# Kernel tuning notes

Measured on AMD Instinct MI355X. Metric: run time of the kernel, lower is better.

## Reference

```python
import jax, jax.numpy as jnp
import numpy as np

B, D, S, H, L = 256, 7, 32, 512, 128  # batch, tree depth, n_symbols, hidden_size, latent_size
N = 2 ** D - 1  # nodes in complete binary tree, heap order (children of i are 2i+1, 2i+2)


def _xavier(key, shape):
    lim = float(np.sqrt(6.0 / (shape[0] + shape[1])))
    return jax.random.uniform(key, shape, jnp.float32, -lim, lim)


def setup_inputs():
    key = jax.random.key(0)
    ks = jax.random.split(key, 18)
    return {
        'symbols': jax.random.randint(ks[0], (B, N), 0, S, dtype=jnp.int32),
        'eps': jax.random.normal(ks[1], (B, L), jnp.float32),
        # Encoder GRU221: gate order [r, z, n], input weights act on one-hot symbol, hidden weights on cat(h_l, h_r)
        'ewi': _xavier(ks[2], (3 * H, S)),
        'ebi': jax.random.uniform(ks[3], (3 * H,), jnp.float32, -0.05, 0.05),
        'ewh': _xavier(ks[4], (3 * H, 2 * H)),
        'ebh': jax.random.uniform(ks[5], (3 * H,), jnp.float32, -0.05, 0.05),
        'h2mu_w': _xavier(ks[6], (L, H)),
        'h2mu_b': jax.random.uniform(ks[7], (L,), jnp.float32, -0.05, 0.05),
        'h2lv_w': _xavier(ks[8], (L, H)),
        'h2lv_b': jax.random.uniform(ks[9], (L,), jnp.float32, -0.05, 0.05),
        # Decoder
        'z2h_w': _xavier(ks[10], (H, L)),
        'z2h_b': jax.random.uniform(ks[11], (H,), jnp.float32, -0.05, 0.05),
        'h2o_w': _xavier(ks[12], (S, H)),
        'h2o_b': jax.random.uniform(ks[13], (S,), jnp.float32, -0.05, 0.05),
        # Decoder GRU122: gate order [r, z, n], each gate has 2H outputs (left/right child)
        'dwi': _xavier(ks[14], (6 * H, S)),
        'dbi': jax.random.uniform(ks[15], (6 * H,), jnp.float32, -0.05, 0.05),
        'dwh': _xavier(ks[16], (6 * H, H)),
        'dbh': jax.random.uniform(ks[17], (6 * H,), jnp.float32, -0.05, 0.05),
    }


def _hvae_forward(symbols, eps, ewi, ebi, ewh, ebh, h2mu_w, h2mu_b, h2lv_w, h2lv_b,
                  z2h_w, z2h_b, h2o_w, h2o_b, dwi, dbi, dwh, dbh):
    x_all = jax.nn.one_hot(symbols, S, dtype=jnp.float32)  # [B, N, S] node targets

    # ---- Encoder: GRU221 applied bottom-up, one batched step per tree level ----
    h = jnp.zeros((B, 2 ** D, H), jnp.float32)  # (absent) children of the deepest level
    for d in range(D - 1, -1, -1):
        n_d = 2 ** d
        x = x_all[:, n_d - 1: 2 * n_d - 1]       # [B, n_d, S] level-d symbols (heap order)
        hl, hr = h[:, 0::2], h[:, 1::2]           # [B, n_d, H] left/right child hiddens
        hcat = jnp.concatenate([hl, hr], axis=-1)
        gi = x @ ewi.T + ebi                       # [B, n_d, 3H]
        gh = hcat @ ewh.T + ebh
        r = jax.nn.sigmoid(gi[..., :H] + gh[..., :H])
        zg = jax.nn.sigmoid(gi[..., H:2 * H] + gh[..., H:2 * H])
        n = jnp.tanh(gi[..., 2 * H:] + r * gh[..., 2 * H:])
        h = (1.0 - zg) * n + zg * (hl + hr) * 0.5
    root = h[:, 0]                                 # [B, H]
    mu = root @ h2mu_w.T + h2mu_b                  # [B, L]
    logvar = root @ h2lv_w.T + h2lv_b
    zlat = mu + eps * jnp.exp(0.5 * logvar)        # reparameterized sample

    # ---- Decoder: GRU122 applied top-down, one batched step per tree level ----
    hidden = (zlat @ z2h_w.T + z2h_b)[:, None, :]  # [B, 1, H] root hidden
    preds = []
    for d in range(D):
        pred = hidden @ h2o_w.T + h2o_b            # [B, 2^d, S]
        preds.append(pred)
        if d < D - 1:
            a = jax.nn.softmax(pred, axis=-1)
            gi = a @ dwi.T + dbi                    # [B, 2^d, 6H]
            gh = hidden @ dwh.T + dbh
            r = jax.nn.sigmoid(gi[..., :2 * H] + gh[..., :2 * H])
            zg = jax.nn.sigmoid(gi[..., 2 * H:4 * H] + gh[..., 2 * H:4 * H])
            n = jnp.tanh(gi[..., 4 * H:] + r * gh[..., 4 * H:])
            dh = jnp.concatenate([hidden, hidden], axis=-1)  # h.repeat(1,1,2)
            out = (1.0 - zg) * n + zg * dh          # [B, 2^d, 2H]
            # torch.split -> (left, right); interleave as next level's hiddens (heap order)
            hidden = jnp.stack([out[..., :H], out[..., H:]], axis=2).reshape(B, 2 ** (d + 1), H)
    preds = jnp.concatenate(preds, axis=1)          # [B, N, S] per-node logits, level order
    return mu, logvar, preds


def reference(symbols, eps, ewi, ebi, ewh, ebh, h2mu_w, h2mu_b, h2lv_w, h2lv_b,
              z2h_w, z2h_b, h2o_w, h2o_b, dwi, dbi, dwh, dbh):
    return _hvae_forward(symbols, eps, ewi, ebi, ewh, ebh, h2mu_w, h2mu_b, h2lv_w, h2lv_b,
                         z2h_w, z2h_b, h2o_w, h2o_b, dwi, dbi, dwh, dbh)
```

## Files before the change

kernel.cpp:

```cpp
#include <hip/hip_runtime.h>
#include <hip/hip_bf16.h>

typedef unsigned short u16;
typedef unsigned int u32;
typedef __attribute__((ext_vector_type(8))) short short8;
typedef __attribute__((ext_vector_type(4))) float f32x4;

#define WAITV(N) asm volatile("s_waitcnt vmcnt(" #N ")" ::: "memory")

__device__ __forceinline__ float sigmoidf_(float x) { return 1.0f / (1.0f + expf(-x)); }

__device__ __forceinline__ float bf2f(u16 u) {
    union { u32 i; float f; } v; v.i = ((u32)u) << 16; return v.f;
}
__device__ __forceinline__ u16 f2bf(float f) {
    union { float f; u32 i; } v; v.f = f;
    u32 lsb = (v.i >> 16) & 1u;
    v.i += 0x7fffu + lsb;
    return (u16)(v.i >> 16);
}

__device__ __forceinline__ void gload16(const u16* g, u16* l) {
    __builtin_amdgcn_global_load_lds(
        (const __attribute__((address_space(1))) u32*)g,
        (__attribute__((address_space(3))) u32*)l, 16, 0, 0);
}

__global__ __launch_bounds__(256) void cvt_bf16(const float* __restrict__ src,
                                                u16* __restrict__ dst, int n)
{
    int i = blockIdx.x * 256 + threadIdx.x;
    if (i < n) dst[i] = f2bf(src[i]);
}

__global__ __launch_bounds__(256) void onehot_k(
    const int* __restrict__ symbols, u16* __restrict__ oneh)
{
    int idx = blockIdx.x * 256 + threadIdx.x;
    int col = idx & 31;
    int row = idx >> 5;
    oneh[idx] = (col == symbols[row]) ? (u16)0x3F80 : (u16)0;
}

__global__ __launch_bounds__(256) void leaf_tab(
    const float* __restrict__ ewi, const float* __restrict__ ebi,
    const float* __restrict__ ebh, u16* __restrict__ tab)
{
    int idx = blockIdx.x * 256 + threadIdx.x;
    int c = idx & 511;
    int sym = idx >> 9;
    float r = sigmoidf_(ewi[c * 32 + sym]          + ebi[c]        + ebh[c]);
    float z = sigmoidf_(ewi[(512 + c) * 32 + sym]  + ebi[512 + c]  + ebh[512 + c]);
    float n = tanhf(    ewi[(1024 + c) * 32 + sym] + ebi[1024 + c] + r * ebh[1024 + c]);
    tab[idx] = f2bf((1.0f - z) * n);
}

__global__ __launch_bounds__(256) void enc_leaf(
    const u16* __restrict__ tab, const int* __restrict__ symbols,
    u16* __restrict__ hout)
{
    int t = blockIdx.x * 256 + threadIdx.x;
    int m = t >> 6, c0 = (t & 63) * 8;
    int sym = symbols[(m >> 6) * 127 + 63 + (m & 63)];
    *reinterpret_cast<short8*>(hout + (size_t)m * 512 + c0) =
        *reinterpret_cast<const short8*>(tab + sym * 512 + c0);
}

template<int RF>
__global__ __launch_bounds__(256, 2) void enc_tile(
    const u16* __restrict__ A, const u16* __restrict__ W,
    const u16* __restrict__ oneh, const u16* __restrict__ Wi,
    const float* __restrict__ ebi, const float* __restrict__ ebh,
    u16* __restrict__ hout, int dlog, int node_base)
{
    constexpr int BM = RF * 32;
    constexpr int NCA = BM / 64;
    constexpr int NS = 32;
    __shared__ alignas(16) u16 Als[4][BM * 32];
    __shared__ alignas(16) u16 Bls[4][192 * 32];
    const int tid  = threadIdx.x;
    const int lane = tid & 63;
    const int wid  = tid >> 6;
    const int wr = wid >> 1, wc = wid & 1;
    const int lr = lane & 15, lk = lane >> 4;
    const int m0 = blockIdx.x * BM;
    const int c0 = blockIdx.y * 64;

    size_t a_goff[NCA]; int a_loff[NCA];
#pragma unroll
    for (int j = 0; j < NCA; ++j) {
        int a = wid * NCA + j;
        int r_ = a * 16 + (lane >> 2);
        int kps = (lane & 3) ^ ((r_ >> 1) & 3);
        a_goff[j] = (size_t)(m0 + r_) * 1024 + kps * 8;
        a_loff[j] = a * 512 + lane * 8;
    }
    size_t b_goff[3]; int b_loff[3];
#pragma unroll
    for (int j = 0; j < 3; ++j) {
        int b = wid * 3 + j;
        int rr = b * 16 + (lane >> 2);
        int kps = (lane & 3) ^ ((rr >> 1) & 3);
        int grow = (rr >> 6) * 512 + c0 + (rr & 63);
        b_goff[j] = (size_t)grow * 1024 + kps * 8;
        b_loff[j] = b * 512 + lane * 8;
    }
    int a_roff[RF];
#pragma unroll
    for (int i = 0; i < RF; ++i) {
        int row = wr * (RF * 16) + i * 16 + lr;
        a_roff[i] = row * 32 + (lk ^ ((row >> 1) & 3)) * 8;
    }
    int b_roff[3][2];
#pragma unroll
    for (int s = 0; s < 3; ++s)
#pragma unroll
        for (int cf = 0; cf < 2; ++cf) {
            int row = s * 64 + wc * 32 + cf * 16 + lr;
            b_roff[s][cf] = row * 32 + (lk ^ ((row >> 1) & 3)) * 8;
        }

    f32x4 acc[4][2][RF];
#pragma unroll
    for (int s = 0; s < 4; ++s)
#pragma unroll
        for (int cf = 0; cf < 2; ++cf)
#pragma unroll
            for (int i = 0; i < RF; ++i) acc[s][cf][i] = (f32x4){0.f, 0.f, 0.f, 0.f};

    auto issue = [&](int stg) {
        const int buf = stg & 3;
        const int nk = stg * 32;
#pragma unroll
        for (int j = 0; j < NCA; ++j) gload16(A + a_goff[j] + nk, &Als[buf][a_loff[j]]);
#pragma unroll
        for (int j = 0; j < 3; ++j) gload16(W + b_goff[j] + nk, &Bls[buf][b_loff[j]]);
    };
    auto compute = [&](int buf) {
        short8 a[RF];
#pragma unroll
        for (int i = 0; i < RF; ++i)
            a[i] = *reinterpret_cast<const short8*>(&Als[buf][a_roff[i]]);
#pragma unroll
        for (int s = 0; s < 3; ++s)
#pragma unroll
            for (int cf = 0; cf < 2; ++cf) {
                short8 b = *reinterpret_cast<const short8*>(&Bls[buf][b_roff[s][cf]]);
#pragma unroll
                for (int i = 0; i < RF; ++i)
                    acc[s][cf][i] = __builtin_amdgcn_mfma_f32_16x16x32_bf16(a[i], b, acc[s][cf][i], 0, 0, 0);
            }
    };

    issue(0); issue(1); issue(2);
    for (int t = 0; t < NS - 2; ++t) {
        if constexpr (RF == 4) WAITV(10); else WAITV(8);
        __builtin_amdgcn_s_barrier();
        if (t + 3 < NS) issue(t + 3);
        compute(t & 3);
    }
    if constexpr (RF == 4) WAITV(5); else WAITV(4);
    __builtin_amdgcn_s_barrier();
    compute((NS - 2) & 3);
    WAITV(0);
    __builtin_amdgcn_s_barrier();
    compute((NS - 1) & 3);

    const int mask = (1 << dlog) - 1;
    {
        short8 oh[RF];
#pragma unroll
        for (int i = 0; i < RF; ++i) {
            int m = m0 + wr * (RF * 16) + i * 16 + lr;
            int b_ = m >> dlog, j_ = m & mask;
            oh[i] = *reinterpret_cast<const short8*>(
                oneh + (size_t)(b_ * 127 + node_base + j_) * 32 + lk * 8);
        }
#pragma unroll
        for (int s = 0; s < 3; ++s) {
            const int d = (s == 2) ? 3 : s;
#pragma unroll
            for (int cf = 0; cf < 2; ++cf) {
                short8 wb = *reinterpret_cast<const short8*>(
                    Wi + (size_t)(s * 512 + c0 + wc * 32 + cf * 16 + lr) * 32 + lk * 8);
#pragma unroll
                for (int i = 0; i < RF; ++i)
                    acc[d][cf][i] = __builtin_amdgcn_mfma_f32_16x16x32_bf16(oh[i], wb, acc[d][cf][i], 0, 0, 0);
            }
        }
    }

    float ebr[2], ebz[2], ebin[2], ebhn[2];
#pragma unroll
    for (int cf = 0; cf < 2; ++cf) {
        int c = c0 + wc * 32 + cf * 16 + lr;
        ebr[cf]  = ebi[c] + ebh[c];
        ebz[cf]  = ebi[512 + c] + ebh[512 + c];
        ebin[cf] = ebi[1024 + c];
        ebhn[cf] = ebh[1024 + c];
    }
#pragma unroll
    for (int i = 0; i < RF; ++i)
#pragma unroll
        for (int r = 0; r < 4; ++r) {
            int m = m0 + wr * (RF * 16) + i * 16 + lk * 4 + r;
#pragma unroll
            for (int cf = 0; cf < 2; ++cf) {
                int c = c0 + wc * 32 + cf * 16 + lr;
                float rr_ = sigmoidf_(acc[0][cf][i][r] + ebr[cf]);
                float zz  = sigmoidf_(acc[1][cf][i][r] + ebz[cf]);
                float nn  = tanhf(acc[3][cf][i][r] + ebin[cf] + rr_ * (acc[2][cf][i][r] + ebhn[cf]));
                float hl = bf2f(A[(size_t)m * 1024 + c]);
                float hr = bf2f(A[(size_t)m * 1024 + 512 + c]);
                hout[(size_t)m * 512 + c] = f2bf((1.0f - zz) * nn + zz * (hl + hr) * 0.5f);
            }
        }
}

__global__ __launch_bounds__(256) void mid1(
    const u16* __restrict__ root, const float* __restrict__ h2mu_w,
    const float* __restrict__ h2mu_b, const float* __restrict__ h2lv_w,
    const float* __restrict__ h2lv_b, const float* __restrict__ eps,
    float* __restrict__ zlat, float* __restrict__ out_mu,
    float* __restrict__ out_lv)
{
    int b = blockIdx.x, t = threadIdx.x;
    __shared__ float rs[512];
    rs[t]       = bf2f(root[(size_t)b * 512 + t]);
    rs[t + 256] = bf2f(root[(size_t)b * 512 + t + 256]);
    __syncthreads();
    const float* w = (t < 128) ? (h2mu_w + (size_t)t * 512) : (h2lv_w + (size_t)(t - 128) * 512);
    float acc = 0.0f;
    for (int k = 0; k < 512; ++k) acc += rs[k] * w[k];
    acc += (t < 128) ? h2mu_b[t] : h2lv_b[t - 128];
    __shared__ float vals[256];
    vals[t] = acc;
    __syncthreads();
    if (t < 128) {
        float mu = vals[t], lv = vals[t + 128];
        float zl = mu + eps[b * 128 + t] * expf(0.5f * lv);
        zlat[b * 128 + t] = zl;
        out_mu[b * 128 + t] = mu;
        out_lv[b * 128 + t] = lv;
    }
}

__global__ __launch_bounds__(512) void mid2(
    const float* __restrict__ zlat, const float* __restrict__ z2h_w,
    const float* __restrict__ z2h_b, u16* __restrict__ hidden)
{
    int b = blockIdx.x, t = threadIdx.x;
    __shared__ float zs[128];
    if (t < 128) zs[t] = zlat[b * 128 + t];
    __syncthreads();
    float acc = z2h_b[t];
    for (int k = 0; k < 128; ++k) acc += zs[k] * z2h_w[(size_t)t * 128 + k];
    hidden[(size_t)b * 512 + t] = f2bf(acc);
}

__global__ __launch_bounds__(256) void pred_mfma(
    const u16* __restrict__ hidden, const u16* __restrict__ Wo,
    const float* __restrict__ h2o_b, u16* __restrict__ aout,
    float* __restrict__ preds_out, int dlog, int node_base, int write_a)
{
    const int lane = threadIdx.x & 63;
    const int wid  = threadIdx.x >> 6;
    const int lr = lane & 15, lk = lane >> 4;
    const int m0 = blockIdx.x * 64 + wid * 16;

    f32x4 acc0 = (f32x4){0.f, 0.f, 0.f, 0.f};
    f32x4 acc1 = (f32x4){0.f, 0.f, 0.f, 0.f};
    const u16* Arow = hidden + (size_t)(m0 + lr) * 512 + lk * 8;
    const u16* B0 = Wo + (size_t)lr * 512 + lk * 8;
    const u16* B1 = Wo + (size_t)(16 + lr) * 512 + lk * 8;
#pragma unroll
    for (int k0 = 0; k0 < 512; k0 += 32) {
        short8 a  = *reinterpret_cast<const short8*>(Arow + k0);
        short8 b0 = *reinterpret_cast<const short8*>(B0 + k0);
        short8 b1 = *reinterpret_cast<const short8*>(B1 + k0);
        acc0 = __builtin_amdgcn_mfma_f32_16x16x32_bf16(a, b0, acc0, 0, 0, 0);
        acc1 = __builtin_amdgcn_mfma_f32_16x16x32_bf16(a, b1, acc1, 0, 0, 0);
    }
    const float bb0 = h2o_b[lr], bb1 = h2o_b[16 + lr];
    const int dmask = (1 << dlog) - 1;
#pragma unroll
    for (int r = 0; r < 4; ++r) {
        float p0 = acc0[r] + bb0;
        float p1 = acc1[r] + bb1;
        float mx = fmaxf(p0, p1);
#pragma unroll
        for (int off = 1; off < 16; off <<= 1) mx = fmaxf(mx, __shfl_xor(mx, off));
        float e0 = expf(p0 - mx), e1 = expf(p1 - mx);
        float s = e0 + e1;
#pragma unroll
        for (int off = 1; off < 16; off <<= 1) s += __shfl_xor(s, off);
        int m = m0 + lk * 4 + r;
        int b_ = m >> dlog, j_ = m & dmask;
        size_t o = (size_t)(b_ * 127 + node_base + j_) * 32;
        preds_out[o + lr] = p0;
        preds_out[o + 16 + lr] = p1;
        if (write_a) {
            float inv = 1.0f / s;
            aout[(size_t)m * 32 + lr]      = f2bf(e0 * inv);
            aout[(size_t)m * 32 + 16 + lr] = f2bf(e1 * inv);
        }
    }
}

template<int RF>
__global__ __launch_bounds__(256, 2) void dec_tile(
    const u16* __restrict__ Hin, const u16* __restrict__ aB,
    const u16* __restrict__ Wh, const u16* __restrict__ Wi,
    const float* __restrict__ dbh, const float* __restrict__ dbi,
    u16* __restrict__ Hout)
{
    constexpr int BM = RF * 32;
    constexpr int NCA = BM / 64;
    constexpr int NS = 16;
    __shared__ alignas(16) u16 Als[4][BM * 32];
    __shared__ alignas(16) u16 Bls[4][192 * 32];
    const int tid  = threadIdx.x;
    const int lane = tid & 63;
    const int wid  = tid >> 6;
    const int wr = wid >> 1, wc = wid & 1;
    const int lr = lane & 15, lk = lane >> 4;
    const int m0 = blockIdx.x * BM;
    const int c0 = blockIdx.y * 64;

    size_t a_goff[NCA]; int a_loff[NCA];
#pragma unroll
    for (int j = 0; j < NCA; ++j) {
        int a = wid * NCA + j;
        int r_ = a * 16 + (lane >> 2);
        int kps = (lane & 3) ^ ((r_ >> 1) & 3);
        a_goff[j] = (size_t)(m0 + r_) * 512 + kps * 8;
        a_loff[j] = a * 512 + lane * 8;
    }
    size_t b_goff[3]; int b_loff[3];
#pragma unroll
    for (int j = 0; j < 3; ++j) {
        int b = wid * 3 + j;
        int rr = b * 16 + (lane >> 2);
        int kps = (lane & 3) ^ ((rr >> 1) & 3);
        int grow = (rr >> 6) * 1024 + c0 + (rr & 63);
        b_goff[j] = (size_t)grow * 512 + kps * 8;
        b_loff[j] = b * 512 + lane * 8;
    }
    int a_roff[RF];
#pragma unroll
    for (int i = 0; i < RF; ++i) {
        int row = wr * (RF * 16) + i * 16 + lr;
        a_roff[i] = row * 32 + (lk ^ ((row >> 1) & 3)) * 8;
    }
    int b_roff[3][2];
#pragma unroll
    for (int s = 0; s < 3; ++s)
#pragma unroll
        for (int cf = 0; cf < 2; ++cf) {
            int row = s * 64 + wc * 32 + cf * 16 + lr;
            b_roff[s][cf] = row * 32 + (lk ^ ((row >> 1) & 3)) * 8;
        }

    f32x4 acc[4][2][RF];
#pragma unroll
    for (int s = 0; s < 4; ++s)
#pragma unroll
        for (int cf = 0; cf < 2; ++cf)
#pragma unroll
            for (int i = 0; i < RF; ++i) acc[s][cf][i] = (f32x4){0.f, 0.f, 0.f, 0.f};

    auto issue = [&](int stg) {
        const int buf = stg & 3;
        const int nk = stg * 32;
#pragma unroll
        for (int j = 0; j < NCA; ++j) gload16(Hin + a_goff[j] + nk, &Als[buf][a_loff[j]]);
#pragma unroll
        for (int j = 0; j < 3; ++j) gload16(Wh + b_goff[j] + nk, &Bls[buf][b_loff[j]]);
    };
    auto compute = [&](int buf) {
        short8 a[RF];
#pragma unroll
        for (int i = 0; i < RF; ++i)
            a[i] = *reinterpret_cast<const short8*>(&Als[buf][a_roff[i]]);
#pragma unroll
        for (int s = 0; s < 3; ++s)
#pragma unroll
            for (int cf = 0; cf < 2; ++cf) {
                short8 b = *reinterpret_cast<const short8*>(&Bls[buf][b_roff[s][cf]]);
#pragma unroll
                for (int i = 0; i < RF; ++i)
                    acc[s][cf][i] = __builtin_amdgcn_mfma_f32_16x16x32_bf16(a[i], b, acc[s][cf][i], 0, 0, 0);
            }
    };

    issue(0); issue(1); issue(2);
    for (int t = 0; t < NS - 2; ++t) {
        if constexpr (RF == 4) WAITV(10); else WAITV(8);
        __builtin_amdgcn_s_barrier();
        if (t + 3 < NS) issue(t + 3);
        compute(t & 3);
    }
    if constexpr (RF == 4) WAITV(5); else WAITV(4);
    __builtin_amdgcn_s_barrier();
    compute((NS - 2) & 3);
    WAITV(0);
    __builtin_amdgcn_s_barrier();
    compute((NS - 1) & 3);

#pragma unroll
    for (int i = 0; i < RF; ++i) {
        short8 aw = *reinterpret_cast<const short8*>(
            aB + (size_t)(m0 + wr * (RF * 16) + i * 16 + lr) * 32 + lk * 8);
#pragma unroll
        for (int s = 0; s < 3; ++s) {
            const int d = (s == 2) ? 3 : s;
#pragma unroll
            for (int cf = 0; cf < 2; ++cf) {
                short8 b = *reinterpret_cast<const short8*>(
                    Wi + (size_t)(s * 1024 + c0 + wc * 32 + cf * 16 + lr) * 32 + lk * 8);
                acc[d][cf][i] = __builtin_amdgcn_mfma_f32_16x16x32_bf16(aw, b, acc[d][cf][i], 0, 0, 0);
            }
        }
    }

#pragma unroll
    for (int i = 0; i < RF; ++i)
#pragma unroll
        for (int r = 0; r < 4; ++r) {
            int m = m0 + wr * (RF * 16) + i * 16 + lk * 4 + r;
#pragma unroll
            for (int cf = 0; cf < 2; ++cf) {
                int c = c0 + wc * 32 + cf * 16 + lr;
                float rr_ = sigmoidf_(acc[0][cf][i][r] + dbh[c]        + dbi[c]);
                float zz  = sigmoidf_(acc[1][cf][i][r] + dbh[1024 + c] + dbi[1024 + c]);
                float nn  = tanhf(acc[3][cf][i][r] + dbi[2048 + c] + rr_ * (acc[2][cf][i][r] + dbh[2048 + c]));
                float hid = bf2f(Hin[(size_t)m * 512 + (c & 511)]);
                Hout[(size_t)m * 1024 + c] = f2bf((1.0f - zz) * nn + zz * hid);
            }
        }
}

extern "C" void kernel_launch(void* const* d_in, const int* in_sizes, int n_in,
                              void* d_out, int out_size, void* d_ws, size_t ws_size,
                              hipStream_t stream) {
    const int*   symbols = (const int*)  d_in[0];
    const float* eps     = (const float*)d_in[1];
    const float* ewi     = (const float*)d_in[2];
    const float* ebi     = (const float*)d_in[3];
    const float* ewh     = (const float*)d_in[4];
    const float* ebh     = (const float*)d_in[5];
    const float* h2mu_w  = (const float*)d_in[6];
    const float* h2mu_b  = (const float*)d_in[7];
    const float* h2lv_w  = (const float*)d_in[8];
    const float* h2lv_b  = (const float*)d_in[9];
    const float* z2h_w   = (const float*)d_in[10];
    const float* z2h_b   = (const float*)d_in[11];
    const float* h2o_w   = (const float*)d_in[12];
    const float* h2o_b   = (const float*)d_in[13];
    const float* dwi     = (const float*)d_in[14];
    const float* dbi     = (const float*)d_in[15];
    const float* dwh     = (const float*)d_in[16];
    const float* dbh     = (const float*)d_in[17];

    float* out    = (float*)d_out;
    float* out_mu = out;
    float* out_lv = out + 256 * 128;
    float* out_pr = out + 2 * 256 * 128;

    u16* bufL  = (u16*)d_ws;
    u16* bufS  = bufL  + (size_t)16384 * 512;
    u16* ewh_b = bufS  + (size_t)8192 * 512;
    u16* dwh_b = ewh_b + (size_t)1536 * 1024;
    u16* dwi_b = dwh_b + (size_t)3072 * 512;
    u16* ewi_b = dwi_b + (size_t)3072 * 32;
    u16* wo_b  = ewi_b + (size_t)1536 * 32;
    u16* ltab  = wo_b  + (size_t)32 * 512;
    u16* oneh  = ltab  + (size_t)32 * 512;
    u16* aBuf  = oneh  + (size_t)32512 * 32;
    float* zlat = (float*)(aBuf + (size_t)8192 * 32);

    cvt_bf16<<<(1572864 + 255) / 256, 256, 0, stream>>>(ewh, ewh_b, 1572864);
    cvt_bf16<<<(1572864 + 255) / 256, 256, 0, stream>>>(dwh, dwh_b, 1572864);
    cvt_bf16<<<(98304 + 255) / 256, 256, 0, stream>>>(dwi, dwi_b, 98304);
    cvt_bf16<<<(49152 + 255) / 256, 256, 0, stream>>>(ewi, ewi_b, 49152);
    cvt_bf16<<<(16384 + 255) / 256, 256, 0, stream>>>(h2o_w, wo_b, 16384);
    onehot_k<<<(32512 * 32) / 256, 256, 0, stream>>>(symbols, oneh);
    leaf_tab<<<64, 256, 0, stream>>>(ewi, ebi, ebh, ltab);

    enc_leaf<<<4096, 256, 0, stream>>>(ltab, symbols, bufL);
    const u16* src = bufL;
    u16*       dst = bufS;
    for (int d = 5; d >= 0; --d) {
        int M = 256 << d;
        if (M >= 8192)
            enc_tile<4><<<dim3(M / 128, 8), 256, 0, stream>>>(src, ewh_b, oneh, ewi_b,
                                                              ebi, ebh, dst, d, (1 << d) - 1);
        else
            enc_tile<2><<<dim3(M / 64, 8), 256, 0, stream>>>(src, ewh_b, oneh, ewi_b,
                                                             ebi, ebh, dst, d, (1 << d) - 1);
        const u16* t = src; src = dst; dst = (u16*)t;
    }
    mid1<<<256, 256, 0, stream>>>(src, h2mu_w, h2mu_b, h2lv_w, h2lv_b, eps, zlat, out_mu, out_lv);
    mid2<<<256, 512, 0, stream>>>(zlat, z2h_w, z2h_b, bufL);

    const u16* hsrc = bufL;
    u16*       hdst = bufS;
    for (int d = 0; d < 6; ++d) {
        int M = 256 << d;
        pred_mfma<<<M / 64, 256, 0, stream>>>(hsrc, wo_b, h2o_b, aBuf, out_pr, d, (1 << d) - 1, 1);
        if (M >= 8192)
            dec_tile<4><<<dim3(M / 128, 16), 256, 0, stream>>>(hsrc, aBuf, dwh_b, dwi_b, dbh, dbi, hdst);
        else
            dec_tile<2><<<dim3(M / 64, 16), 256, 0, stream>>>(hsrc, aBuf, dwh_b, dwi_b, dbh, dbi, hdst);
        const u16* t = hsrc; hsrc = hdst; hdst = (u16*)t;
    }
    pred_mfma<<<16384 / 64, 256, 0, stream>>>(hsrc, wo_b, h2o_b, aBuf, out_pr, 6, 63, 0);
}
```

Baseline: 414.5 us.

## Merge prep kernels and fuse leaf-table gather into first encoder level

Folds the five weight-conversion launches, the one-hot builder and the leaf-table builder into a single prep kernel, which cuts launch overhead. It also removes the enc_leaf kernel: the first internal encoder level now gathers its children's hidden states straight from the 32-row leaf table, indexed by symbol, instead of reading a materialized 16384x512 buffer. This saves a large write and read of leaf hiddens. The cost is per-row symbol lookups inside the GEMM tile and a branchy flattened prep kernel.

```diff
diff --git a/kernel.cpp b/kernel.cpp
--- a/kernel.cpp
+++ b/kernel.cpp
@@ -26,50 +26,46 @@
         (__attribute__((address_space(3))) u32*)l, 16, 0, 0);
 }
 
-__global__ __launch_bounds__(256) void cvt_bf16(const float* __restrict__ src,
-                                                u16* __restrict__ dst, int n)
-{
-    int i = blockIdx.x * 256 + threadIdx.x;
-    if (i < n) dst[i] = f2bf(src[i]);
-}
-
-__global__ __launch_bounds__(256) void onehot_k(
-    const int* __restrict__ symbols, u16* __restrict__ oneh)
+__global__ __launch_bounds__(256) void prep(
+    const float* __restrict__ ewh, const float* __restrict__ dwh,
+    const float* __restrict__ dwi, const float* __restrict__ ewi,
+    const float* __restrict__ h2o_w, const int* __restrict__ symbols,
+    const float* __restrict__ ebi, const float* __restrict__ ebh,
+    u16* __restrict__ ewh_b, u16* __restrict__ dwh_b, u16* __restrict__ dwi_b,
+    u16* __restrict__ ewi_b, u16* __restrict__ wo_b, u16* __restrict__ oneh,
+    u16* __restrict__ ltab)
 {
     int idx = blockIdx.x * 256 + threadIdx.x;
-    int col = idx & 31;
-    int row = idx >> 5;
-    oneh[idx] = (col == symbols[row]) ? (u16)0x3F80 : (u16)0;
-}
-
-__global__ __launch_bounds__(256) void leaf_tab(
-    const float* __restrict__ ewi, const float* __restrict__ ebi,
-    const float* __restrict__ ebh, u16* __restrict__ tab)
-{
-    int idx = blockIdx.x * 256 + threadIdx.x;
-    int c = idx & 511;
-    int sym = idx >> 9;
-    float r = sigmoidf_(ewi[c * 32 + sym]          + ebi[c]        + ebh[c]);
-    float z = sigmoidf_(ewi[(512 + c) * 32 + sym]  + ebi[512 + c]  + ebh[512 + c]);
-    float n = tanhf(    ewi[(1024 + c) * 32 + sym] + ebi[1024 + c] + r * ebh[1024 + c]);
-    tab[idx] = f2bf((1.0f - z) * n);
-}
-
-__global__ __launch_bounds__(256) void enc_leaf(
-    const u16* __restrict__ tab, const int* __restrict__ symbols,
-    u16* __restrict__ hout)
-{
-    int t = blockIdx.x * 256 + threadIdx.x;
-    int m = t >> 6, c0 = (t & 63) * 8;
-    int sym = symbols[(m >> 6) * 127 + 63 + (m & 63)];
-    *reinterpret_cast<short8*>(hout + (size_t)m * 512 + c0) =
-        *reinterpret_cast<const short8*>(tab + sym * 512 + c0);
-}
-
-template<int RF>
+    if (idx < 1572864) { ewh_b[idx] = f2bf(ewh[idx]); return; }
+    idx -= 1572864;
+    if (idx < 1572864) { dwh_b[idx] = f2bf(dwh[idx]); return; }
+    idx -= 1572864;
+    if (idx < 98304) { dwi_b[idx] = f2bf(dwi[idx]); return; }
+    idx -= 98304;
+    if (idx < 49152) { ewi_b[idx] = f2bf(ewi[idx]); return; }
+    idx -= 49152;
+    if (idx < 16384) { wo_b[idx] = f2bf(h2o_w[idx]); return; }
+    idx -= 16384;
+    if (idx < 1040384) {
+        int col = idx & 31, row = idx >> 5;
+        oneh[idx] = (col == symbols[row]) ? (u16)0x3F80 : (u16)0;
+        return;
+    }
+    idx -= 1040384;
+    if (idx < 16384) {
+        int c = idx & 511, sym = idx >> 9;
+        float r = sigmoidf_(ewi[c * 32 + sym]          + ebi[c]        + ebh[c]);
+        float z = sigmoidf_(ewi[(512 + c) * 32 + sym]  + ebi[512 + c]  + ebh[512 + c]);
+        float n = tanhf(    ewi[(1024 + c) * 32 + sym] + ebi[1024 + c] + r * ebh[1024 + c]);
+        ltab[idx] = f2bf((1.0f - z) * n);
+    }
+}
+
+template<int RF, bool LEAF>
 __global__ __launch_bounds__(256, 2) void enc_tile(
     const u16* __restrict__ A, const u16* __restrict__ W,
     const u16* __restrict__ oneh, const u16* __restrict__ Wi,
+    const u16* __restrict__ tab, const int* __restrict__ symbols,
     const float* __restrict__ ebi, const float* __restrict__ ebh,
     u16* __restrict__ hout, int dlog, int node_base)
 {
@@ -85,15 +81,27 @@
     const int lr = lane & 15, lk = lane >> 4;
     const int m0 = blockIdx.x * BM;
     const int c0 = blockIdx.y * 64;
+    const int mask = (1 << dlog) - 1;
 
     size_t a_goff[NCA]; int a_loff[NCA];
+    int symL[NCA], symR[NCA];
 #pragma unroll
     for (int j = 0; j < NCA; ++j) {
         int a = wid * NCA + j;
         int r_ = a * 16 + (lane >> 2);
         int kps = (lane & 3) ^ ((r_ >> 1) & 3);
-        a_goff[j] = (size_t)(m0 + r_) * 1024 + kps * 8;
         a_loff[j] = a * 512 + lane * 8;
+        if constexpr (LEAF) {
+            int rg = m0 + r_;
+            int b_ = rg >> dlog, jj = rg & mask;
+            int cbase = b_ * 127 + 2 * (node_base + jj) + 1;
+            symL[j] = symbols[cbase];
+            symR[j] = symbols[cbase + 1];
+            a_goff[j] = kps * 8;
+        } else {
+            a_goff[j] = (size_t)(m0 + r_) * 1024 + kps * 8;
+            symL[j] = symR[j] = 0;
+        }
     }
     size_t b_goff[3]; int b_loff[3];
 #pragma unroll
@@ -132,7 +140,16 @@
         const int buf = stg & 3;
         const int nk = stg * 32;
 #pragma unroll
-        for (int j = 0; j < NCA; ++j) gload16(A + a_goff[j] + nk, &Als[buf][a_loff[j]]);
+        for (int j = 0; j < NCA; ++j) {
+            if constexpr (LEAF) {
+                const u16* src = (nk < 512)
+                    ? tab + (size_t)symL[j] * 512 + nk + a_goff[j]
+                    : tab + (size_t)symR[j] * 512 + (nk - 512) + a_goff[j];
+                gload16(src, &Als[buf][a_loff[j]]);
+            } else {
+                gload16(A + a_goff[j] + nk, &Als[buf][a_loff[j]]);
+            }
+        }
 #pragma unroll
         for (int j = 0; j < 3; ++j) gload16(W + b_goff[j] + nk, &Bls[buf][b_loff[j]]);
     };
@@ -166,7 +183,6 @@
     __builtin_amdgcn_s_barrier();
     compute((NS - 1) & 3);
 
-    const int mask = (1 << dlog) - 1;
     {
         short8 oh[RF];
 #pragma unroll
@@ -204,14 +220,27 @@
 #pragma unroll
         for (int r = 0; r < 4; ++r) {
             int m = m0 + wr * (RF * 16) + i * 16 + lk * 4 + r;
+            int symLm = 0, symRm = 0;
+            if constexpr (LEAF) {
+                int b_ = m >> dlog, jj = m & mask;
+                int cbase = b_ * 127 + 2 * (node_base + jj) + 1;
+                symLm = symbols[cbase];
+                symRm = symbols[cbase + 1];
+            }
 #pragma unroll
             for (int cf = 0; cf < 2; ++cf) {
                 int c = c0 + wc * 32 + cf * 16 + lr;
                 float rr_ = sigmoidf_(acc[0][cf][i][r] + ebr[cf]);
                 float zz  = sigmoidf_(acc[1][cf][i][r] + ebz[cf]);
                 float nn  = tanhf(acc[3][cf][i][r] + ebin[cf] + rr_ * (acc[2][cf][i][r] + ebhn[cf]));
-                float hl = bf2f(A[(size_t)m * 1024 + c]);
-                float hr = bf2f(A[(size_t)m * 1024 + 512 + c]);
+                float hl, hr;
+                if constexpr (LEAF) {
+                    hl = bf2f(tab[(size_t)symLm * 512 + c]);
+                    hr = bf2f(tab[(size_t)symRm * 512 + c]);
+                } else {
+                    hl = bf2f(A[(size_t)m * 1024 + c]);
+                    hr = bf2f(A[(size_t)m * 1024 + 512 + c]);
+                }
                 hout[(size_t)m * 512 + c] = f2bf((1.0f - zz) * nn + zz * (hl + hr) * 0.5f);
             }
         }
@@ -479,25 +508,18 @@
     u16* aBuf  = oneh  + (size_t)32512 * 32;
     float* zlat = (float*)(aBuf + (size_t)8192 * 32);
 
-    cvt_bf16<<<(1572864 + 255) / 256, 256, 0, stream>>>(ewh, ewh_b, 1572864);
-    cvt_bf16<<<(1572864 + 255) / 256, 256, 0, stream>>>(dwh, dwh_b, 1572864);
-    cvt_bf16<<<(98304 + 255) / 256, 256, 0, stream>>>(dwi, dwi_b, 98304);
-    cvt_bf16<<<(49152 + 255) / 256, 256, 0, stream>>>(ewi, ewi_b, 49152);
-    cvt_bf16<<<(16384 + 255) / 256, 256, 0, stream>>>(h2o_w, wo_b, 16384);
-    onehot_k<<<(32512 * 32) / 256, 256, 0, stream>>>(symbols, oneh);
-    leaf_tab<<<64, 256, 0, stream>>>(ewi, ebi, ebh, ltab);
-
-    enc_leaf<<<4096, 256, 0, stream>>>(ltab, symbols, bufL);
-    const u16* src = bufL;
-    u16*       dst = bufS;
-    for (int d = 5; d >= 0; --d) {
+    prep<<<(4366336 + 255) / 256, 256, 0, stream>>>(
+        ewh, dwh, dwi, ewi, h2o_w, symbols, ebi, ebh,
+        ewh_b, dwh_b, dwi_b, ewi_b, wo_b, oneh, ltab);
+
+    enc_tile<4, true><<<dim3(64, 8), 256, 0, stream>>>(
+        nullptr, ewh_b, oneh, ewi_b, ltab, symbols, ebi, ebh, bufS, 5, 31);
+    const u16* src = bufS;
+    u16*       dst = bufL;
+    for (int d = 4; d >= 0; --d) {
         int M = 256 << d;
-        if (M >= 8192)
-            enc_tile<4><<<dim3(M / 128, 8), 256, 0, stream>>>(src, ewh_b, oneh, ewi_b,
-                                                              ebi, ebh, dst, d, (1 << d) - 1);
-        else
-            enc_tile<2><<<dim3(M / 64, 8), 256, 0, stream>>>(src, ewh_b, oneh, ewi_b,
-                                                             ebi, ebh, dst, d, (1 << d) - 1);
+        enc_tile<2, false><<<dim3(M / 64, 8), 256, 0, stream>>>(
+            src, ewh_b, oneh, ewi_b, ltab, symbols, ebi, ebh, dst, d, (1 << d) - 1);
         const u16* t = src; src = dst; dst = (u16*)t;
     }
     mid1<<<256, 256, 0, stream>>>(src, h2mu_w, h2mu_b, h2lv_w, h2lv_b, eps, zlat, out_mu, out_lv);
```

Measured after the change: 393.7 us. -5.0%, faster.
